# Optimization experiments

Hardware: AMD Instinct MI355X
Metric: run time of the kernel (lower is better)

Reference implementation:

```python
import jax, jax.numpy as jnp
import numpy as np

B, L, C = 128, 512, 321
PRED = 336
S = 4
K = 25  # moving_avg kernel
EPS = 1e-5
N = L // S          # 128
H = 2048 // S       # 512


def setup_inputs() -> dict:
    key = jax.random.key(0)
    ks = jax.random.split(key, 16)
    def w(k, shape, fan_in):
        return jax.random.uniform(k, shape, jnp.float32, -1.0, 1.0) / np.sqrt(fan_in)
    return {
        "x": jax.random.normal(ks[0], (B, L, C), jnp.float32),
        "revin_w": jnp.ones((C,), jnp.float32),
        "revin_b": jnp.zeros((C,), jnp.float32),
        "W11": w(ks[1], (N, H), N), "b11": w(ks[2], (H,), N),
        "W12": w(ks[3], (H, N), H), "b12": w(ks[4], (N,), H),
        "W21": w(ks[5], (N, H), N), "b21": w(ks[6], (H,), N),
        "W22": w(ks[7], (H, N), H), "b22": w(ks[8], (N,), H),
        "W_tr": w(ks[9], (L, PRED), L), "b_tr": w(ks[10], (PRED,), L),
        "W_se": w(ks[11], (L, PRED), L), "b_se": w(ks[12], (PRED,), L),
    }


def reference(x, revin_w, revin_b, W11, b11, W12, b12, W21, b21, W22, b22,
              W_tr, b_tr, W_se, b_se):
    # RevIN norm (statistics are detached in the original)
    mean = jax.lax.stop_gradient(jnp.mean(x, axis=1, keepdims=True))
    std = jax.lax.stop_gradient(
        jnp.sqrt(jnp.var(x, axis=1, keepdims=True) + EPS))
    xn = (x - mean) / std * revin_w + revin_b  # [B, L, C]

    # Decomp: replicate-pad along time then moving average of width K
    front = jnp.repeat(xn[:, 0:1, :], K - 1 - (K - 1) // 2, axis=1)
    end = jnp.repeat(xn[:, -1:, :], (K - 1) // 2, axis=1)
    padded = jnp.concatenate([front, xn, end], axis=1)  # [B, L+K-1, C]
    cs = jnp.concatenate(
        [jnp.zeros((B, 1, C), padded.dtype), jnp.cumsum(padded, axis=1)], axis=1)
    trend = (cs[:, K:, :] - cs[:, :-K, :]) / K  # [B, L, C]
    seasonal = xn - trend

    trend_p = jnp.transpose(trend, (0, 2, 1))      # [B, C, L]
    seasonal_p = jnp.transpose(seasonal, (0, 2, 1))  # [B, C, L]

    # Trend head: Linear L -> PRED
    trend_out = jnp.einsum('bcl,lp->bcp', trend_p, W_tr) + b_tr

    # Seasonal head: Splitting (strided interleave) = reshape + transpose
    xs = seasonal_p.reshape(B, C, N, S).transpose(0, 1, 3, 2)  # [B, C, S, N]
    h = jnp.matmul(jax.nn.gelu(jnp.matmul(xs, W11) + b11, approximate=False), W12) + b12
    h = jnp.matmul(jax.nn.gelu(jnp.matmul(h, W21) + b21, approximate=False), W22) + b22
    # Catting is the exact inverse interleave
    sea = h.transpose(0, 1, 3, 2).reshape(B, C, L)  # [B, C, L]
    sea_out = jnp.einsum('bcl,lp->bcp', sea, W_se) + b_se

    out = jnp.transpose(trend_out + sea_out, (0, 2, 1))  # [B, PRED, C]

    # RevIN denorm
    out = (out - revin_b) / (revin_w + EPS * EPS)
    out = out * std + mean
    return out
```

## Files before the change

### kernel.cpp

```cpp
#include <hip/hip_runtime.h>
#include <math.h>

#define BB   128
#define LL   512
#define CC   321
#define PREDD 336

using bf16x8  = __attribute__((ext_vector_type(8))) __bf16;
using floatx4 = __attribute__((ext_vector_type(4))) float;
using uintx4  = __attribute__((ext_vector_type(4))) unsigned int;
typedef unsigned short u16;
typedef unsigned int u32;

#define MFMA16(a,b,c) __builtin_amdgcn_mfma_f32_16x16x32_bf16(a,b,c,0,0,0)

__device__ __forceinline__ u16 f2bf(float f){
    union { float f; unsigned u; } v; v.f = f;
    unsigned r = v.u + 0x7FFFu + ((v.u >> 16) & 1u);
    return (u16)(r >> 16);
}

__device__ __forceinline__ float fgelu(float x){
    float u = x*(0.7978845608f + 0.035677408f*x*x);
    float a = fminf(u*2.8853900818f, 80.f);
    float t = __builtin_amdgcn_exp2f(a);
    return x*t*__builtin_amdgcn_rcpf(1.f + t);
}

__device__ __forceinline__ int swz128(int r, int s){ return r*128 + (((s & 8) | ((s ^ r) & 7)) << 3); }
__device__ __forceinline__ int swz64 (int r, int s){ return r*64  + (((s ^ r) & 7) << 3); }

__device__ __forceinline__ void dma16(const u16* g, const u16* l){
    __builtin_amdgcn_global_load_lds(
        (const __attribute__((address_space(1))) u32*)g,
        (__attribute__((address_space(3))) u32*)l, 16, 0, 0);
}

__global__ void prep_k(const float* __restrict__ W11, const float* __restrict__ W12,
                       const float* __restrict__ W21, const float* __restrict__ W22,
                       const float* __restrict__ Wtr, const float* __restrict__ Wse,
                       u16* __restrict__ BT1, u16* __restrict__ BT2,
                       u16* __restrict__ BT3, u16* __restrict__ BT4,
                       u16* __restrict__ BT5)
{
    int idx = blockIdx.x * 256 + threadIdx.x;
    if (idx < 65536){
        int h = idx >> 7, k = idx & 127;
        BT1[idx] = f2bf(W11[k*512 + h]);
        BT3[idx] = f2bf(W21[k*512 + h]);
        int n = idx >> 9, k2 = idx & 511;
        BT2[idx] = f2bf(W12[k2*128 + n]);
        BT4[idx] = f2bf(W22[k2*128 + n]);
    }
    if (idx < 393216){
        int p = idx >> 10, k = idx & 1023;
        float v = 0.f;
        if (p < PREDD){
            if (k < 512) v = Wtr[k*PREDD + p];
            else { int kk = k - 512; int s = kk >> 7; int n = kk & 127; v = Wse[(4*n + s)*PREDD + p]; }
        }
        BT5[idx] = f2bf(v);
    }
}

#define XT(t,c) xt[((t)<<4) + (((t)>>5)<<1) + (c)]
__global__ __launch_bounds__(256) void decomp_k(
    const float* __restrict__ x, const float* __restrict__ rw, const float* __restrict__ rb,
    u16* __restrict__ Afin, u16* __restrict__ xs, float2* __restrict__ stats)
{
    __shared__ float xt[8240];
    __shared__ float red[2][16][16];
    __shared__ float sh_m[16], sh_istd[16];
    int b = blockIdx.x / 21, ct = blockIdx.x % 21;
    int tid = threadIdx.x;

    int cl = tid & 15, lp = tid >> 4;
    int c = ct*16 + cl;
    bool valid = c < CC;
    const float* xb = x + (size_t)b*LL*CC;
    float s = 0.f, q = 0.f;
    for (int i = 0; i < 32; ++i){
        int t = lp + 16*i;
        float v = valid ? xb[(size_t)t*CC + c] : 0.f;
        XT(t, cl) = v;
        s += v; q += v*v;
    }
    red[0][lp][cl] = s; red[1][lp][cl] = q;
    __syncthreads();
    if (tid < 16){
        float ss = 0.f, qq = 0.f;
        for (int j = 0; j < 16; ++j){ ss += red[0][j][tid]; qq += red[1][j][tid]; }
        float m  = ss * (1.f/512.f);
        float var = qq * (1.f/512.f) - m*m;
        float sd = sqrtf(var + 1e-5f);
        sh_m[tid] = m; sh_istd[tid] = 1.f/sd;
        int cc = ct*16 + tid;
        if (cc < CC) stats[(size_t)b*CC + cc] = make_float2(m, sd);
    }
    __syncthreads();

    int ch = tid >> 4, tp = tid & 15;
    int c2 = ct*16 + ch;
    if (c2 >= CC) return;
    float m = sh_m[ch], istd = sh_istd[ch];
    float w = rw[c2] * istd, bbv = rb[c2];
    size_t bc = (size_t)b*CC + c2;
    u16* tr  = Afin + bc*1024;
    u16* xsr = xs   + bc*512;
    int t0 = tp*32;

    float win = 0.f;
#pragma unroll
    for (int d = -12; d <= 12; ++d){
        int u = t0 + d; u = u < 0 ? 0 : (u > 511 ? 511 : u);
        win += XT(u, ch);
    }
    u16 trbuf[8];
    u16 xsbuf[4][8];
#pragma unroll
    for (int i = 0; i < 32; ++i){
        int t = t0 + i;
        float Ax = win * (1.f/25.f);
        float xv = XT(t, ch);
        trbuf[i & 7] = f2bf((Ax - m)*w + bbv);
        xsbuf[i & 3][i >> 2] = f2bf((xv - Ax)*w);
        if ((i & 7) == 7)
            *(uintx4*)(tr + t0 + (i & ~7)) = *(const uintx4*)trbuf;
        int uo = t - 12; uo = uo < 0 ? 0 : uo;
        int un = t + 13; un = un > 511 ? 511 : un;
        win += XT(un, ch) - XT(uo, ch);
    }
#pragma unroll
    for (int s4 = 0; s4 < 4; ++s4)
        *(uintx4*)(xsr + s4*128 + tp*8) = *(const uintx4*)xsbuf[s4];
}

#define SL1 16384
#define HS  32768
__global__ __launch_bounds__(256, 2) void mlp_fused_k(
    const u16* __restrict__ xs,
    const u16* __restrict__ BT1, const float* __restrict__ b11,
    const u16* __restrict__ BT2, const float* __restrict__ b12,
    const u16* __restrict__ BT3, const float* __restrict__ b21,
    const u16* __restrict__ BT4, const float* __restrict__ b22,
    u16* __restrict__ Afin)
{
    __shared__ u16 lds[40960];
    const int tid = threadIdx.x;
    const int row0 = blockIdx.x * 128;
    const int lane = tid & 63;
    const int wv = tid >> 6;
    const int quad = lane >> 4, cl = lane & 15;
    const int wrow = row0 + wv*32;
    u16* hscr = lds + HS + wv*2048;
    const int rdswz = ((cl >> 2) & 3) << 4;

#pragma unroll
    for (int i = 0; i < 4; ++i){
        int qq = (wv*4 + i)*64 + lane;
        { int r = qq >> 4, sp = qq & 15; int s = (sp & 8) | ((sp ^ r) & 7);
          dma16(BT1 + (size_t)r*128 + s*8, lds + qq*8); }
        { int r = qq >> 3, p = qq & 7; int s = (p ^ r) & 7;
          dma16(BT2 + (size_t)r*512 + s*8, lds + 8192 + qq*8); }
    }
    bf16x8 afrag[2][4];
#pragma unroll
    for (int mt = 0; mt < 2; ++mt)
#pragma unroll
        for (int ks = 0; ks < 4; ++ks)
            afrag[mt][ks] = *(const bf16x8*)(xs + (size_t)(wrow + mt*16 + cl)*128 + ks*32 + quad*8);

    floatx4 Yacc[16];
#pragma unroll
    for (int i = 0; i < 16; ++i) Yacc[i] = (floatx4){0.f,0.f,0.f,0.f};

    __syncthreads();

    for (int g = 0; g < 16; ++g){
        const int cur = (g & 1) ? SL1 : 0;
        const int nxt = (g & 1) ? 0 : SL1;
        if (g < 15){
            const u16* w1s = ((g+1) & 8) ? BT3 : BT1;
            const u16* w2s = ((g+1) & 8) ? BT4 : BT2;
            const int hb = ((g+1) & 7) * 64;
#pragma unroll
            for (int i = 0; i < 4; ++i){
                int qq = (wv*4 + i)*64 + lane;
                { int r = qq >> 4, sp = qq & 15; int s = (sp & 8) | ((sp ^ r) & 7);
                  dma16(w1s + (size_t)(hb + r)*128 + s*8, lds + nxt + qq*8); }
                { int r = qq >> 3, p = qq & 7; int s = (p ^ r) & 7;
                  dma16(w2s + (size_t)r*512 + hb + s*8, lds + nxt + 8192 + qq*8); }
            }
        }
        const float* ba = (g & 8) ? b21 : b11;
        const int hc = g & 7;

        floatx4 hacc[8];
#pragma unroll
        for (int i = 0; i < 8; ++i) hacc[i] = (floatx4){0.f,0.f,0.f,0.f};
#pragma unroll
        for (int ks = 0; ks < 4; ++ks){
            bf16x8 bfr[4];
#pragma unroll
            for (int nt = 0; nt < 4; ++nt)
                bfr[nt] = *(const bf16x8*)(lds + cur + swz128(nt*16 + cl, ks*4 + quad));
#pragma unroll
            for (int mt = 0; mt < 2; ++mt)
#pragma unroll
                for (int nt = 0; nt < 4; ++nt)
                    hacc[mt*4+nt] = MFMA16(afrag[mt][ks], bfr[nt], hacc[mt*4+nt]);
        }
#pragma unroll
        for (int mt = 0; mt < 2; ++mt)
#pragma unroll
            for (int nt = 0; nt < 4; ++nt){
                floatx4 v = hacc[mt*4+nt];
                int h = nt*16 + cl;
                float bav = ba[hc*64 + h];
#pragma unroll
                for (int i = 0; i < 4; ++i){
                    int r = mt*16 + quad*4 + i;
                    hscr[r*64 + (h ^ (quad << 4))] = f2bf(fgelu(v[i] + bav));
                }
            }
#pragma unroll
        for (int ks = 0; ks < 2; ++ks){
            bf16x8 a2[2];
#pragma unroll
            for (int mt = 0; mt < 2; ++mt)
                a2[mt] = *(const bf16x8*)(hscr + (mt*16 + cl)*64 + ((ks*32 + quad*8) ^ rdswz));
#pragma unroll
            for (int nt = 0; nt < 8; ++nt){
                bf16x8 b2 = *(const bf16x8*)(lds + cur + 8192 + swz64(nt*16 + cl, ks*4 + quad));
#pragma unroll
                for (int mt = 0; mt < 2; ++mt)
                    Yacc[mt*8+nt] = MFMA16(a2[mt], b2, Yacc[mt*8+nt]);
            }
        }
        __syncthreads();

        if (g == 7){
#pragma unroll
            for (int half = 0; half < 2; ++half){
#pragma unroll
                for (int mt = 0; mt < 2; ++mt)
#pragma unroll
                    for (int nt = 0; nt < 4; ++nt){
                        int ntg = half*4 + nt;
                        floatx4 v = Yacc[mt*8+ntg];
                        int c = ntg*16 + cl;
                        float bv = b12[c];
                        int h = nt*16 + cl;
#pragma unroll
                        for (int i = 0; i < 4; ++i){
                            int r = mt*16 + quad*4 + i;
                            hscr[r*64 + (h ^ (quad << 4))] = f2bf(v[i] + bv);
                        }
                    }
#pragma unroll
                for (int mt = 0; mt < 2; ++mt)
#pragma unroll
                    for (int k2 = 0; k2 < 2; ++k2)
                        afrag[mt][half*2 + k2] = *(const bf16x8*)(hscr + (mt*16 + cl)*64 + ((k2*32 + quad*8) ^ rdswz));
            }
#pragma unroll
            for (int i = 0; i < 16; ++i) Yacc[i] = (floatx4){0.f,0.f,0.f,0.f};
        }
    }

#pragma unroll
    for (int mt = 0; mt < 2; ++mt)
#pragma unroll
        for (int nt = 0; nt < 8; ++nt){
            int c = nt*16 + cl;
            float bv = b22[c];
            floatx4 v = Yacc[mt*8+nt];
#pragma unroll
            for (int i = 0; i < 4; ++i){
                int gr = wrow + mt*16 + quad*4 + i;
                Afin[(size_t)(gr>>2)*1024 + 512 + (size_t)(gr&3)*128 + c] = f2bf(v[i] + bv);
            }
        }
}

__global__ __launch_bounds__(256, 2) void head_gemm_k(
    const u16* __restrict__ A, const u16* __restrict__ BT,
    float* __restrict__ Cf,
    const float* __restrict__ bias, const float* __restrict__ bias2,
    const float* __restrict__ rw, const float* __restrict__ rb,
    const float2* __restrict__ stats)
{
    __shared__ u16 lds[32768];
    const int id = blockIdx.x;
    const int xcd = id & 7, slot = id >> 3;
    const int g8 = slot / 3, j = slot - g8*3;
    const int by = xcd + 8*g8;
    if (by >= 321) return;
    const int row0 = by * 128, col0 = j * 128;

    const int tid = threadIdx.x;
    const int lane = tid & 63;
    const int wv = tid >> 6;
    const int wm = wv & 1, wn = wv >> 1;
    const int quad = lane >> 4, cl = lane & 15;

    const int qbase = wv*4*64 + lane;

#pragma unroll
    for (int i = 0; i < 4; ++i){
        int qq = qbase + i*64;
        int r = qq >> 3, p = qq & 7; int s = (p ^ r) & 7;
        dma16(A  + (size_t)(row0 + r)*1024 + s*8, lds + qq*8);
        dma16(BT + (size_t)(col0 + r)*1024 + s*8, lds + 16384 + qq*8);
    }
    __syncthreads();

    floatx4 acc[16];
#pragma unroll
    for (int i = 0; i < 16; ++i) acc[i] = (floatx4){0.f,0.f,0.f,0.f};

    for (int it = 0; it < 16; ++it){
        const int cur = (it & 1) * 8192;
        if (it < 15){
            const int nxt = ((it+1) & 1) * 8192;
            const int k0 = (it+1) * 64;
#pragma unroll
            for (int i = 0; i < 4; ++i){
                int qq = qbase + i*64;
                int r = qq >> 3, p = qq & 7; int s = (p ^ r) & 7;
                dma16(A  + (size_t)(row0 + r)*1024 + k0 + s*8, lds + nxt + qq*8);
                dma16(BT + (size_t)(col0 + r)*1024 + k0 + s*8, lds + 16384 + nxt + qq*8);
            }
        }
#pragma unroll
        for (int kk = 0; kk < 2; ++kk){
            bf16x8 af[4], bfr[4];
#pragma unroll
            for (int mt = 0; mt < 4; ++mt) af[mt]  = *(const bf16x8*)(lds + cur + swz64(wm*64 + mt*16 + cl, kk*4 + quad));
#pragma unroll
            for (int nt = 0; nt < 4; ++nt) bfr[nt] = *(const bf16x8*)(lds + 16384 + cur + swz64(wn*64 + nt*16 + cl, kk*4 + quad));
#pragma unroll
            for (int mt = 0; mt < 4; ++mt)
#pragma unroll
                for (int nt = 0; nt < 4; ++nt)
                    acc[mt*4+nt] = MFMA16(af[mt], bfr[nt], acc[mt*4+nt]);
        }
        __syncthreads();
    }

#pragma unroll
    for (int mt = 0; mt < 4; ++mt)
#pragma unroll
        for (int nt = 0; nt < 4; ++nt){
            floatx4 v = acc[mt*4+nt];
            int gc = col0 + wn*64 + nt*16 + cl;
            if (gc >= PREDD) continue;
            float bsum = bias[gc] + bias2[gc];
#pragma unroll
            for (int i = 0; i < 4; ++i){
                int gr = row0 + wm*64 + mt*16 + quad*4 + i;
                float val = v[i] + bsum;
                int bv2 = gr / CC;
                int c  = gr - bv2*CC;
                val = (val - rb[c]) / (rw[c] + 1e-10f);
                float2 st = stats[gr];
                val = val*st.y + st.x;
                Cf[(size_t)bv2*(PREDD*CC) + (size_t)gc*CC + c] = val;
            }
        }
}

extern "C" void kernel_launch(void* const* d_in, const int* in_sizes, int n_in,
                              void* d_out, int out_size, void* d_ws, size_t ws_size,
                              hipStream_t stream)
{
    const float* x   = (const float*)d_in[0];
    const float* rvw = (const float*)d_in[1];
    const float* rvb = (const float*)d_in[2];
    const float* W11 = (const float*)d_in[3];
    const float* b11 = (const float*)d_in[4];
    const float* W12 = (const float*)d_in[5];
    const float* b12 = (const float*)d_in[6];
    const float* W21 = (const float*)d_in[7];
    const float* b21 = (const float*)d_in[8];
    const float* W22 = (const float*)d_in[9];
    const float* b22 = (const float*)d_in[10];
    const float* Wtr = (const float*)d_in[11];
    const float* btr = (const float*)d_in[12];
    const float* Wse = (const float*)d_in[13];
    const float* bse = (const float*)d_in[14];
    float* out = (float*)d_out;

    char* ws = (char*)d_ws;
    u16* BT1 = (u16*)(ws + 0);
    u16* BT2 = (u16*)(ws + 131072);
    u16* BT3 = (u16*)(ws + 262144);
    u16* BT4 = (u16*)(ws + 393216);
    u16* BT5 = (u16*)(ws + 524288);
    float2* stats = (float2*)(ws + 1310720);
    u16* Afin = (u16*)(ws + 1639424);
    u16* xs   = (u16*)(ws + 85787648);

    hipLaunchKernelGGL(prep_k, dim3(1536), dim3(256), 0, stream,
                       W11, W12, W21, W22, Wtr, Wse, BT1, BT2, BT3, BT4, BT5);
    hipLaunchKernelGGL(decomp_k, dim3(128*21), dim3(256), 0, stream,
                       x, rvw, rvb, Afin, xs, stats);
    hipLaunchKernelGGL(mlp_fused_k, dim3(1284), dim3(256), 0, stream,
                       xs, BT1, b11, BT2, b12, BT3, b21, BT4, b22, Afin);
    hipLaunchKernelGGL(head_gemm_k, dim3(984), dim3(256), 0, stream,
                       Afin, BT5, out, btr, bse, rvw, rvb, stats);
}
```

Measured before the change: 451.2 us.

## Shrink MLP hidden chunk to 32, transpose MFMA operands, raise occupancy to 3 waves

Measured after the change: 460.8 us. 1.02x slower.

```diff
diff --git a/kernel.cpp b/kernel.cpp
--- a/kernel.cpp
+++ b/kernel.cpp
@@ -9,6 +9,7 @@
 using bf16x8  = __attribute__((ext_vector_type(8))) __bf16;
 using floatx4 = __attribute__((ext_vector_type(4))) float;
 using uintx4  = __attribute__((ext_vector_type(4))) unsigned int;
+using uintx2  = __attribute__((ext_vector_type(2))) unsigned int;
 typedef unsigned short u16;
 typedef unsigned int u32;
 
@@ -19,16 +20,21 @@
     unsigned r = v.u + 0x7FFFu + ((v.u >> 16) & 1u);
     return (u16)(r >> 16);
 }
+__device__ __forceinline__ u32 pack2bf(float a, float b){
+    union { float f; u32 u; } x, y; x.f = a; y.f = b;
+    u32 lo = (x.u + 0x7FFFu + ((x.u >> 16) & 1u)) >> 16;
+    u32 hi = (y.u + 0x7FFFu + ((y.u >> 16) & 1u)) & 0xFFFF0000u;
+    return hi | lo;
+}
 
 __device__ __forceinline__ float fgelu(float x){
     float u = x*(0.7978845608f + 0.035677408f*x*x);
-    float a = fminf(u*2.8853900818f, 80.f);
-    float t = __builtin_amdgcn_exp2f(a);
-    return x*t*__builtin_amdgcn_rcpf(1.f + t);
-}
-
-__device__ __forceinline__ int swz128(int r, int s){ return r*128 + (((s & 8) | ((s ^ r) & 7)) << 3); }
-__device__ __forceinline__ int swz64 (int r, int s){ return r*64  + (((s ^ r) & 7) << 3); }
+    float na = fminf(-2.8853900818f*u, 80.f);
+    float t = __builtin_amdgcn_exp2f(na);
+    return x*__builtin_amdgcn_rcpf(1.f + t);
+}
+
+__device__ __forceinline__ int swz64(int r, int s){ return r*64 + (((s ^ r) & 7) << 3); }
 
 __device__ __forceinline__ void dma16(const u16* g, const u16* l){
     __builtin_amdgcn_global_load_lds(
@@ -135,9 +141,33 @@
         *(uintx4*)(xsr + s4*128 + tp*8) = *(const uintx4*)xsbuf[s4];
 }
 
-#define SL1 16384
-#define HS  32768
-__global__ __launch_bounds__(256, 2) void mlp_fused_k(
+#define SCR 16384
+__device__ __forceinline__ void stage_chunk(u16* lds, int slot,
+    const u16* w1s, const u16* w2s, int hb, int wv, int lane)
+{
+#pragma unroll
+    for (int i = 0; i < 2; ++i){
+        int qq = (wv*2 + i)*64 + lane;
+        int h = qq >> 4, sp = qq & 15;
+        int s = (sp & 8) | ((sp ^ h) & 7);
+        dma16(w1s + (size_t)(hb + h)*128 + s*8, lds + slot + qq*8);
+        int kh = qq >> 8, n = (qq >> 1) & 127, s1 = qq & 1;
+        int s2 = s1 ^ (n & 1);
+        dma16(w2s + (size_t)n*512 + hb + kh*16 + s2*8, lds + slot + 4096 + qq*8);
+    }
+}
+__device__ __forceinline__ void wr_h(u16* hscr, int grp, int rt, int cl, u32 lo, u32 hi){
+    *(uintx2*)(hscr + (rt*16 + cl)*32 + (((grp ^ (cl & 7)) << 2))) = (uintx2){lo, hi};
+}
+__device__ __forceinline__ bf16x8 rd_h(const u16* hscr, int rt, int quad, int cl){
+    int a0 = (rt*16 + cl)*32 + (((2*quad) ^ (cl & 7)) << 2);
+    union { bf16x8 v; uintx2 p[2]; } u;
+    u.p[0] = *(const uintx2*)(hscr + a0);
+    u.p[1] = *(const uintx2*)(hscr + (a0 ^ 4));
+    return u.v;
+}
+
+__global__ __launch_bounds__(256, 3) void mlp_fused_k(
     const u16* __restrict__ xs,
     const u16* __restrict__ BT1, const float* __restrict__ b11,
     const u16* __restrict__ BT2, const float* __restrict__ b12,
@@ -145,123 +175,97 @@
     const u16* __restrict__ BT4, const float* __restrict__ b22,
     u16* __restrict__ Afin)
 {
-    __shared__ u16 lds[40960];
+    __shared__ u16 lds[20480];
     const int tid = threadIdx.x;
     const int row0 = blockIdx.x * 128;
     const int lane = tid & 63;
     const int wv = tid >> 6;
     const int quad = lane >> 4, cl = lane & 15;
     const int wrow = row0 + wv*32;
-    u16* hscr = lds + HS + wv*2048;
-    const int rdswz = ((cl >> 2) & 3) << 4;
-
-#pragma unroll
-    for (int i = 0; i < 4; ++i){
-        int qq = (wv*4 + i)*64 + lane;
-        { int r = qq >> 4, sp = qq & 15; int s = (sp & 8) | ((sp ^ r) & 7);
-          dma16(BT1 + (size_t)r*128 + s*8, lds + qq*8); }
-        { int r = qq >> 3, p = qq & 7; int s = (p ^ r) & 7;
-          dma16(BT2 + (size_t)r*512 + s*8, lds + 8192 + qq*8); }
-    }
+    u16* hscr = lds + SCR + wv*1024;
+
     bf16x8 afrag[2][4];
 #pragma unroll
-    for (int mt = 0; mt < 2; ++mt)
+    for (int rt = 0; rt < 2; ++rt)
 #pragma unroll
         for (int ks = 0; ks < 4; ++ks)
-            afrag[mt][ks] = *(const bf16x8*)(xs + (size_t)(wrow + mt*16 + cl)*128 + ks*32 + quad*8);
+            afrag[rt][ks] = *(const bf16x8*)(xs + (size_t)(wrow + rt*16 + cl)*128 + ks*32 + quad*8);
+
+    stage_chunk(lds, 0, BT1, BT2, 0, wv, lane);
 
     floatx4 Yacc[16];
 #pragma unroll
     for (int i = 0; i < 16; ++i) Yacc[i] = (floatx4){0.f,0.f,0.f,0.f};
+    floatx4 hacc[4];
 
     __syncthreads();
 
-    for (int g = 0; g < 16; ++g){
-        const int cur = (g & 1) ? SL1 : 0;
-        const int nxt = (g & 1) ? 0 : SL1;
-        if (g < 15){
-            const u16* w1s = ((g+1) & 8) ? BT3 : BT1;
-            const u16* w2s = ((g+1) & 8) ? BT4 : BT2;
-            const int hb = ((g+1) & 7) * 64;
-#pragma unroll
-            for (int i = 0; i < 4; ++i){
-                int qq = (wv*4 + i)*64 + lane;
-                { int r = qq >> 4, sp = qq & 15; int s = (sp & 8) | ((sp ^ r) & 7);
-                  dma16(w1s + (size_t)(hb + r)*128 + s*8, lds + nxt + qq*8); }
-                { int r = qq >> 3, p = qq & 7; int s = (p ^ r) & 7;
-                  dma16(w2s + (size_t)r*512 + hb + s*8, lds + nxt + 8192 + qq*8); }
-            }
-        }
-        const float* ba = (g & 8) ? b21 : b11;
-        const int hc = g & 7;
-
-        floatx4 hacc[8];
-#pragma unroll
-        for (int i = 0; i < 8; ++i) hacc[i] = (floatx4){0.f,0.f,0.f,0.f};
-#pragma unroll
-        for (int ks = 0; ks < 4; ++ks){
-            bf16x8 bfr[4];
-#pragma unroll
-            for (int nt = 0; nt < 4; ++nt)
-                bfr[nt] = *(const bf16x8*)(lds + cur + swz128(nt*16 + cl, ks*4 + quad));
-#pragma unroll
-            for (int mt = 0; mt < 2; ++mt)
-#pragma unroll
-                for (int nt = 0; nt < 4; ++nt)
-                    hacc[mt*4+nt] = MFMA16(afrag[mt][ks], bfr[nt], hacc[mt*4+nt]);
-        }
-#pragma unroll
-        for (int mt = 0; mt < 2; ++mt)
-#pragma unroll
-            for (int nt = 0; nt < 4; ++nt){
-                floatx4 v = hacc[mt*4+nt];
-                int h = nt*16 + cl;
-                float bav = ba[hc*64 + h];
-#pragma unroll
-                for (int i = 0; i < 4; ++i){
-                    int r = mt*16 + quad*4 + i;
-                    hscr[r*64 + (h ^ (quad << 4))] = f2bf(fgelu(v[i] + bav));
+    for (int g = 0; g < 32; ++g){
+        const int cur = (g & 1) * 8192;
+        if (g < 31){
+            const u16* w1s = ((g+1) & 16) ? BT3 : BT1;
+            const u16* w2s = ((g+1) & 16) ? BT4 : BT2;
+            stage_chunk(lds, 8192 - cur, w1s, w2s, ((g+1) & 15)*32, wv, lane);
+        }
+        const float* ba = (g & 16) ? b21 : b11;
+        const int hoff = (g & 15) * 32;
+
+#pragma unroll
+        for (int i = 0; i < 4; ++i) hacc[i] = (floatx4){0.f,0.f,0.f,0.f};
+#pragma unroll
+        for (int ks = 0; ks < 4; ++ks)
+#pragma unroll
+            for (int ht = 0; ht < 2; ++ht){
+                int h = ht*16 + cl;
+                int s = ks*4 + quad;
+                int sp = (s & 8) | ((s ^ h) & 7);
+                bf16x8 w1f = *(const bf16x8*)(lds + cur + h*128 + sp*8);
+                hacc[ht*2+0] = MFMA16(w1f, afrag[0][ks], hacc[ht*2+0]);
+                hacc[ht*2+1] = MFMA16(w1f, afrag[1][ks], hacc[ht*2+1]);
+            }
+#pragma unroll
+        for (int ht = 0; ht < 2; ++ht){
+            floatx4 bv = *(const floatx4*)(ba + hoff + ht*16 + quad*4);
+#pragma unroll
+            for (int rt = 0; rt < 2; ++rt){
+                floatx4 v = hacc[ht*2+rt];
+                wr_h(hscr, ht*4 + quad, rt, cl,
+                     pack2bf(fgelu(v[0]+bv[0]), fgelu(v[1]+bv[1])),
+                     pack2bf(fgelu(v[2]+bv[2]), fgelu(v[3]+bv[3])));
+            }
+        }
+        {
+            bf16x8 hfr0 = rd_h(hscr, 0, quad, cl);
+            bf16x8 hfr1 = rd_h(hscr, 1, quad, cl);
+#pragma unroll
+            for (int nt = 0; nt < 8; ++nt){
+                int n = nt*16 + cl;
+                bf16x8 w2f = *(const bf16x8*)(lds + cur + 4096 + (quad >> 1)*2048
+                                              + n*16 + (((quad & 1) ^ (n & 1)) << 3));
+                Yacc[nt*2+0] = MFMA16(w2f, hfr0, Yacc[nt*2+0]);
+                Yacc[nt*2+1] = MFMA16(w2f, hfr1, Yacc[nt*2+1]);
+            }
+        }
+        __syncthreads();
+
+        if (g == 15){
+#pragma unroll
+            for (int np = 0; np < 4; ++np){
+#pragma unroll
+                for (int nt2 = 0; nt2 < 2; ++nt2){
+                    int nt = np*2 + nt2;
+                    floatx4 bv = *(const floatx4*)(b12 + nt*16 + quad*4);
+#pragma unroll
+                    for (int rt = 0; rt < 2; ++rt){
+                        floatx4 v = Yacc[nt*2+rt];
+                        wr_h(hscr, nt2*4 + quad, rt, cl,
+                             pack2bf(v[0]+bv[0], v[1]+bv[1]),
+                             pack2bf(v[2]+bv[2], v[3]+bv[3]));
+                    }
                 }
-            }
-#pragma unroll
-        for (int ks = 0; ks < 2; ++ks){
-            bf16x8 a2[2];
-#pragma unroll
-            for (int mt = 0; mt < 2; ++mt)
-                a2[mt] = *(const bf16x8*)(hscr + (mt*16 + cl)*64 + ((ks*32 + quad*8) ^ rdswz));
-#pragma unroll
-            for (int nt = 0; nt < 8; ++nt){
-                bf16x8 b2 = *(const bf16x8*)(lds + cur + 8192 + swz64(nt*16 + cl, ks*4 + quad));
-#pragma unroll
-                for (int mt = 0; mt < 2; ++mt)
-                    Yacc[mt*8+nt] = MFMA16(a2[mt], b2, Yacc[mt*8+nt]);
-            }
-        }
-        __syncthreads();
-
-        if (g == 7){
-#pragma unroll
-            for (int half = 0; half < 2; ++half){
-#pragma unroll
-                for (int mt = 0; mt < 2; ++mt)
-#pragma unroll
-                    for (int nt = 0; nt < 4; ++nt){
-                        int ntg = half*4 + nt;
-                        floatx4 v = Yacc[mt*8+ntg];
-                        int c = ntg*16 + cl;
-                        float bv = b12[c];
-                        int h = nt*16 + cl;
-#pragma unroll
-                        for (int i = 0; i < 4; ++i){
-                            int r = mt*16 + quad*4 + i;
-                            hscr[r*64 + (h ^ (quad << 4))] = f2bf(v[i] + bv);
-                        }
-                    }
-#pragma unroll
-                for (int mt = 0; mt < 2; ++mt)
-#pragma unroll
-                    for (int k2 = 0; k2 < 2; ++k2)
-                        afrag[mt][half*2 + k2] = *(const bf16x8*)(hscr + (mt*16 + cl)*64 + ((k2*32 + quad*8) ^ rdswz));
+#pragma unroll
+                for (int rt = 0; rt < 2; ++rt)
+                    afrag[rt][np] = rd_h(hscr, rt, quad, cl);
             }
 #pragma unroll
             for (int i = 0; i < 16; ++i) Yacc[i] = (floatx4){0.f,0.f,0.f,0.f};
@@ -269,21 +273,22 @@
     }
 
 #pragma unroll
-    for (int mt = 0; mt < 2; ++mt)
+    for (int rt = 0; rt < 2; ++rt){
+        int gr = wrow + rt*16 + cl;
+        size_t base = (size_t)(gr >> 2)*1024 + 512 + (size_t)(gr & 3)*128;
 #pragma unroll
         for (int nt = 0; nt < 8; ++nt){
-            int c = nt*16 + cl;
-            float bv = b22[c];
-            floatx4 v = Yacc[mt*8+nt];
-#pragma unroll
-            for (int i = 0; i < 4; ++i){
-                int gr = wrow + mt*16 + quad*4 + i;
-                Afin[(size_t)(gr>>2)*1024 + 512 + (size_t)(gr&3)*128 + c] = f2bf(v[i] + bv);
-            }
-        }
-}
-
-__global__ __launch_bounds__(256, 2) void head_gemm_k(
+            int c0 = nt*16 + quad*4;
+            floatx4 bv = *(const floatx4*)(b22 + c0);
+            floatx4 v = Yacc[nt*2+rt];
+            uintx2 pk = { pack2bf(v[0]+bv[0], v[1]+bv[1]),
+                          pack2bf(v[2]+bv[2], v[3]+bv[3]) };
+            *(uintx2*)(Afin + base + c0) = pk;
+        }
+    }
+}
+
+__global__ __launch_bounds__(256, 3) void head_gemm_k(
     const u16* __restrict__ A, const u16* __restrict__ BT,
     float* __restrict__ Cf,
     const float* __restrict__ bias, const float* __restrict__ bias2,
```
